# Performance work log

Measured on AMD Instinct MI355X. Metric: run time of the kernel, lower is better.

The kernel has to match this reference:

```python
import jax, jax.numpy as jnp
import numpy as np

N = 262144
C = 4096  # number of clusters


def _segment_max(x, seg, num_segments):
    # global_max_pool: per-cluster max over points
    return jax.ops.segment_max(x, seg, num_segments=num_segments)


def setup_inputs() -> dict:
    key = jax.random.key(0)
    ks = jax.random.split(key, 16)

    def lin(k, fan_in, fan_out):
        bound = 1.0 / np.sqrt(fan_in)
        kw, kb = jax.random.split(k)
        W = jax.random.uniform(kw, (fan_in, fan_out), jnp.float32, -bound, bound)
        b = jax.random.uniform(kb, (fan_out,), jnp.float32, -bound, bound)
        return W, b

    relative_points = jax.random.normal(ks[0], (N, 3), jnp.float32)
    features = jax.random.normal(ks[1], (N, 64), jnp.float32)
    cluster = jax.random.randint(ks[2], (N,), 0, C, jnp.int64)

    enc_W1, enc_b1 = lin(ks[3], 3, 32)    # neighborhood encoder MLP
    enc_W2, enc_b2 = lin(ks[4], 32, 64)
    W1, b1 = lin(ks[5], 3 + 64 + 64, 128)  # fc_layers (input_size + enc_out + 3)
    W2, b2 = lin(ks[6], 128, 128)
    G1, gb1 = lin(ks[7], 128, 128)          # fc_layers_global
    G2, gb2 = lin(ks[8], 128, 256)

    return dict(relative_points=relative_points, features=features, cluster=cluster,
                enc_W1=enc_W1, enc_b1=enc_b1, enc_W2=enc_W2, enc_b2=enc_b2,
                W1=W1, b1=b1, W2=W2, b2=b2, G1=G1, gb1=gb1, G2=G2, gb2=gb2)


def reference(relative_points, features, cluster,
              enc_W1, enc_b1, enc_W2, enc_b2,
              W1, b1, W2, b2, G1, gb1, G2, gb2):
    # --- neighborhood encoder: per-point MLP then per-cluster max-pool ---
    h = jax.nn.relu(relative_points @ enc_W1 + enc_b1)          # [N, 32]
    h = jax.nn.relu(h @ enc_W2 + enc_b2)                        # [N, 64]
    neigh_enc = _segment_max(h, cluster, C)                     # [C, 64]

    # gather-by-index duplication + concat
    dup = neigh_enc[cluster]                                    # [N, 64]
    encoded = jnp.concatenate([relative_points, features, dup], axis=1)  # [N, 131]

    # local fc stack (relu, leaky=False)
    encoded = jax.nn.relu(encoded @ W1 + b1)                    # [N, 128]
    encoded = jax.nn.relu(encoded @ W2 + b2)                    # [N, 128]

    # global_max_pool (mean=False)
    encoded_global = _segment_max(encoded, cluster, C)          # [C, 128]

    # global fc stack
    encoded_global = jax.nn.relu(encoded_global @ G1 + gb1)     # [C, 128]
    encoded_global = jax.nn.relu(encoded_global @ G2 + gb2)     # [C, 256]
    return encoded_global
```

## Files before the change

### kernel.cpp

```cpp
#include <hip/hip_runtime.h>
#include <hip/hip_bf16.h>

#define NN 262144
#define CC 4096
#define NBLK 64
#define PPB (NN / NBLK)
#define NT (NN / 64)
#define SLOTS 3

typedef __attribute__((ext_vector_type(8))) short bf16x8;
typedef __attribute__((ext_vector_type(4))) float f32x4;

__device__ __forceinline__ unsigned pk2(float a, float b) {
  __hip_bfloat16 ha = __float2bfloat16(a);
  __hip_bfloat16 hb = __float2bfloat16(b);
  unsigned short ua, ub;
  __builtin_memcpy(&ua, &ha, 2);
  __builtin_memcpy(&ub, &hb, 2);
  return (unsigned)ua | ((unsigned)ub << 16);
}

__global__ __launch_bounds__(256) void k_init(
    const int* __restrict__ cluster, unsigned* __restrict__ hist2d,
    const float* __restrict__ eW2, const float* __restrict__ W1,
    const float* __restrict__ W2, unsigned* __restrict__ packE,
    unsigned* __restrict__ pack1, unsigned* __restrict__ pack2)
{
  __shared__ unsigned h[CC];
  const int t = threadIdx.x, b = blockIdx.x;
  if (b < NBLK) {
    for (int q = t; q < CC; q += 256) h[q] = 0u;
    __syncthreads();
    const int base = b * PPB;
#pragma unroll 4
    for (int k = 0; k < PPB; k += 256) atomicAdd(&h[cluster[base + k + t]], 1u);
    __syncthreads();
    for (int q = t; q < CC; q += 256) hist2d[b * CC + q] = h[q];
    return;
  }
  const int id = (b - NBLK) * 256 + t;
  if (id < 1024) {
    const int nt = id >> 8, l = (id >> 2) & 63, v = id & 3;
    const int k0 = (l >> 4) * 8 + 2 * v, col = nt * 16 + (l & 15);
    packE[id] = pk2(eW2[k0 * 64 + col], eW2[(k0 + 1) * 64 + col]);
  } else if (id < 1024 + 6144) {
    const int j = id - 1024;
    const int kk = j >> 11, nt = (j >> 8) & 7, l = (j >> 2) & 63, v = j & 3;
    const int col = nt * 16 + (l & 15);
    float vals[2];
#pragma unroll
    for (int hh = 0; hh < 2; ++hh) {
      const int k = kk * 32 + (l >> 4) * 8 + 2 * v + hh;
      vals[hh] = (k < 64) ? W1[(3 + k) * 128 + col]
               : (k < 67) ? W1[(k - 64) * 128 + col] : 0.f;
    }
    pack1[j] = pk2(vals[0], vals[1]);
  } else {
    const int j = id - (1024 + 6144);
    const int kk = j >> 11, nt = (j >> 8) & 7, l = (j >> 2) & 63, v = j & 3;
    const int col = nt * 16 + (l & 15);
    const int k0 = kk * 32 + (l >> 4) * 4 + v;
    pack2[j] = pk2(W2[k0 * 128 + col], W2[(k0 + 16) * 128 + col]);
  }
}

#define ZERO_F4 589824
__global__ __launch_bounds__(256) void k_scan_a(
    const unsigned* __restrict__ hist2d, unsigned* __restrict__ base2d,
    unsigned* __restrict__ totals, float4* __restrict__ zbase)
{
  const int t = threadIdx.x, b = blockIdx.x;
  if (b < 16) {
    const int c = b * 256 + t;
    unsigned acc = 0;
#pragma unroll 4
    for (int bb = 0; bb < NBLK; ++bb) {
      const unsigned v = hist2d[bb * CC + c];
      base2d[bb * CC + c] = acc;
      acc += v;
    }
    totals[c] = acc;
  } else {
    const int zb = b - 16;
    const float4 z = {0.f, 0.f, 0.f, 0.f};
#pragma unroll 5
    for (int q = 0; q < 25; ++q) {
      const int idx = (zb * 25 + q) * 256 + t;
      if (idx < ZERO_F4) zbase[idx] = z;
    }
  }
}

__global__ __launch_bounds__(256) void k_scatter(
    const int* __restrict__ cluster, const unsigned* __restrict__ base2d,
    const unsigned* __restrict__ totals, unsigned* __restrict__ permcid,
    unsigned* __restrict__ cstart_g)
{
  __shared__ unsigned cur[CC];
  __shared__ unsigned part[256];
  const int t = threadIdx.x, b = blockIdx.x;
  unsigned loc[16];
  unsigned s = 0;
#pragma unroll
  for (int q = 0; q < 16; ++q) { loc[q] = s; s += totals[t * 16 + q]; }
  part[t] = s;
  __syncthreads();
  for (int off = 1; off < 256; off <<= 1) {
    const unsigned v = (t >= off) ? part[t - off] : 0u;
    __syncthreads();
    part[t] += v;
    __syncthreads();
  }
  const unsigned baset = part[t] - s;
#pragma unroll
  for (int q = 0; q < 16; ++q) {
    const unsigned cs = baset + loc[q];
    cur[t * 16 + q] = base2d[b * CC + t * 16 + q] + cs;
    if (b == 0) cstart_g[t * 16 + q] = cs;
  }
  __syncthreads();
  const int base = b * PPB;
#pragma unroll 4
  for (int k = 0; k < PPB; k += 256) {
    const int i = base + k + t;
    const int c = cluster[i];
    const unsigned pos = atomicAdd(&cur[c], 1u);
    permcid[pos] = (unsigned)i | ((unsigned)c << 18);
  }
}

__global__ __launch_bounds__(256) void k_enc_t(
    const float* __restrict__ pts, const unsigned* __restrict__ permcid,
    const unsigned* __restrict__ cstart,
    const float* __restrict__ eW1, const float* __restrict__ eb1,
    const float* __restrict__ eb2, const unsigned* __restrict__ packE,
    float* __restrict__ pse)
{
  __shared__ float P4[64 * 4];
  __shared__ unsigned h1s[64 * 20];
  __shared__ int seg_r0[65];
  __shared__ int seg_cid[64];
  __shared__ int seg_j[64];
  __shared__ int nseg_s;
  const int t = threadIdx.x;
  const int lane = t & 63, w = t >> 6;
  const int g = lane >> 4, ln15 = lane & 15;
  const int b = blockIdx.x;

  if (w == 0) {
    const unsigned pc = permcid[b * 64 + t];
    const int cid = (int)(pc >> 18);
    const int prevcid = (t == 0) ? -1 : (int)(permcid[b * 64 + t - 1] >> 18);
    const bool flag = (t == 0) || (prevcid != cid);
    const unsigned long long mask = __ballot(flag);
    const int rank = (int)__popcll(mask & ((1ull << t) - 1ull));
    if (flag) {
      seg_r0[rank] = t;
      seg_cid[rank] = cid;
      seg_j[rank] = b - (int)(cstart[cid] >> 6);
    }
    if (t == 0) {
      const int ns = (int)__popcll(mask);
      nseg_s = ns;
      seg_r0[ns] = 64;
    }
    const int i = (int)(pc & 0x3FFFFu);
    P4[t * 4 + 0] = pts[i * 3 + 0];
    P4[t * 4 + 1] = pts[i * 3 + 1];
    P4[t * 4 + 2] = pts[i * 3 + 2];
    P4[t * 4 + 3] = 0.f;
  }
  __syncthreads();
  {
    const int r = t >> 2, qq = t & 3;
    const float p0 = P4[r * 4], p1 = P4[r * 4 + 1], p2 = P4[r * 4 + 2];
    unsigned wv[4];
#pragma unroll
    for (int u = 0; u < 4; ++u) {
      float hv[2];
#pragma unroll
      for (int hh = 0; hh < 2; ++hh) {
        const int cc2 = qq * 8 + 2 * u + hh;
        hv[hh] = fmaxf(fmaf(p2, eW1[64 + cc2],
                       fmaf(p1, eW1[32 + cc2],
                       fmaf(p0, eW1[cc2], eb1[cc2]))), 0.f);
      }
      wv[u] = pk2(hv[0], hv[1]);
    }
    uint4 st; st.x = wv[0]; st.y = wv[1]; st.z = wv[2]; st.w = wv[3];
    *reinterpret_cast<uint4*>(&h1s[r * 20 + qq * 4]) = st;
  }
  __syncthreads();
  {
    const int col = w * 16 + ln15;
    const bf16x8 bfr = *reinterpret_cast<const bf16x8*>(&packE[(w * 64 + lane) * 4]);
    const float bias = eb2[col];
    f32x4 acc[4];
#pragma unroll
    for (int m = 0; m < 4; ++m) acc[m] = f32x4{bias, bias, bias, bias};
#pragma unroll
    for (int m = 0; m < 4; ++m) {
      const bf16x8 a = *reinterpret_cast<const bf16x8*>(&h1s[(16 * m + ln15) * 20 + g * 4]);
      acc[m] = __builtin_amdgcn_mfma_f32_16x16x32_bf16(a, bfr, acc[m], 0, 0, 0);
    }
    const int nseg = nseg_s;
    for (int s = 0; s < nseg; ++s) {
      const int r0 = seg_r0[s], r1 = seg_r0[s + 1];
      float v = 0.f;
#pragma unroll
      for (int m = 0; m < 4; ++m)
#pragma unroll
        for (int q = 0; q < 4; ++q) {
          const int row = 16 * m + 4 * g + q;
          const bool in = (row >= r0) & (row < r1);
          v = fmaxf(v, in ? fmaxf(acc[m][q], 0.f) : 0.f);
        }
      v = fmaxf(v, __shfl_xor(v, 16, 64));
      v = fmaxf(v, __shfl_xor(v, 32, 64));
      if (lane < 16) {
        const int c = seg_cid[s], j = seg_j[s];
        if (j < SLOTS - 1)
          pse[((size_t)c * SLOTS + j) * 64 + col] = v;
        else
          atomicMax((int*)&pse[((size_t)c * SLOTS + (SLOTS - 1)) * 64 + col],
                    __float_as_int(v));
      }
    }
  }
}

__global__ __launch_bounds__(256) void k_cproj2(
    const float* __restrict__ pse, const float* __restrict__ W1,
    const float* __restrict__ b1, float* __restrict__ cproj)
{
  __shared__ float nm2[2][64];
  const int t = threadIdx.x, b = blockIdx.x;
  if (t < 128) {
    const int rr = t >> 6, col = t & 63;
    const float* p = pse + ((size_t)(b * 2 + rr) * SLOTS) * 64 + col;
    nm2[rr][col] = fmaxf(fmaxf(p[0], p[64]), p[128]);
  }
  __syncthreads();
  const int rr = t >> 7, col = t & 127;
  const float* __restrict__ Wd = W1 + 67 * 128;
  float a = b1[col];
#pragma unroll 4
  for (int j = 0; j < 16; ++j) {
    const f32x4 nv = *reinterpret_cast<const f32x4*>(&nm2[rr][4 * j]);
    a = fmaf(nv[0], Wd[(4 * j + 0) * 128 + col], a);
    a = fmaf(nv[1], Wd[(4 * j + 1) * 128 + col], a);
    a = fmaf(nv[2], Wd[(4 * j + 2) * 128 + col], a);
    a = fmaf(nv[3], Wd[(4 * j + 3) * 128 + col], a);
  }
  cproj[(size_t)(b * 2 + rr) * 128 + col] = a;
}

__global__ __launch_bounds__(256) void k_fc_t(
    const float* __restrict__ pts, const float* __restrict__ feat,
    const unsigned* __restrict__ permcid, const unsigned* __restrict__ cstart,
    const float* __restrict__ b2, const float* __restrict__ cproj,
    const unsigned* __restrict__ pack1, const unsigned* __restrict__ pack2,
    float* __restrict__ psf)
{
  __shared__ unsigned buf[64 * 68];
  __shared__ float cpd[8][128];
  __shared__ int ridx_l[64];
  __shared__ int cid_l[64];
  __shared__ int seg_r0[65];
  __shared__ int seg_cid[64];
  __shared__ int seg_j[64];
  __shared__ int nseg_s;
  const int t = threadIdx.x;
  const int lane = t & 63, w = t >> 6;
  const int g = lane >> 4, ln15 = lane & 15;
  const int b = blockIdx.x;

  if (w == 0) {
    const unsigned pc = permcid[b * 64 + t];
    const int cid = (int)(pc >> 18);
    cid_l[t] = cid;
    const int prevcid = (t == 0) ? -1 : (int)(permcid[b * 64 + t - 1] >> 18);
    const bool flag = (t == 0) || (prevcid != cid);
    const unsigned long long mask = __ballot(flag);
    const int rank = (int)__popcll(mask & ((1ull << t) - 1ull));
    ridx_l[t] = (int)__popcll(mask & ((2ull << t) - 1ull)) - 1;
    if (flag) {
      seg_r0[rank] = t;
      seg_cid[rank] = cid;
      seg_j[rank] = b - (int)(cstart[cid] >> 6);
    }
    if (t == 0) {
      const int ns = (int)__popcll(mask);
      nseg_s = ns;
      seg_r0[ns] = 64;
    }
  }
  {
    const int r = t >> 2, seg = t & 3;
    const int i = (int)(permcid[b * 64 + r] & 0x3FFFFu);
    const float4* __restrict__ fp = reinterpret_cast<const float4*>(&feat[(size_t)i * 64 + seg * 16]);
    const float4 f0 = fp[0], f1 = fp[1], f2 = fp[2], f3 = fp[3];
    uint4 s0v, s1v;
    s0v.x = pk2(f0.x, f0.y); s0v.y = pk2(f0.z, f0.w);
    s0v.z = pk2(f1.x, f1.y); s0v.w = pk2(f1.z, f1.w);
    s1v.x = pk2(f2.x, f2.y); s1v.y = pk2(f2.z, f2.w);
    s1v.z = pk2(f3.x, f3.y); s1v.w = pk2(f3.z, f3.w);
    *reinterpret_cast<uint4*>(&buf[r * 52 + seg * 8 + 0]) = s0v;
    *reinterpret_cast<uint4*>(&buf[r * 52 + seg * 8 + 4]) = s1v;
  }
  if (t < 64) {
    const int i = (int)(permcid[b * 64 + t] & 0x3FFFFu);
    uint4 pw;
    pw.x = pk2(pts[i * 3 + 0], pts[i * 3 + 1]);
    pw.y = pk2(pts[i * 3 + 2], 0.f);
    pw.z = 0u; pw.w = 0u;
    uint4 zz; zz.x = zz.y = zz.z = zz.w = 0u;
    *reinterpret_cast<uint4*>(&buf[t * 52 + 32]) = pw;
    *reinterpret_cast<uint4*>(&buf[t * 52 + 36]) = zz;
    *reinterpret_cast<uint4*>(&buf[t * 52 + 40]) = zz;
    *reinterpret_cast<uint4*>(&buf[t * 52 + 44]) = zz;
  }
  __syncthreads();
  {
    const int nseg = nseg_s;
    const int lim = (nseg < 8) ? nseg : 8;
    for (int s = t >> 7; s < lim; s += 2)
      cpd[s][t & 127] = cproj[(size_t)seg_cid[s] * 128 + (t & 127)];
  }
  __syncthreads();

  const int colA = w * 32 + ln15, colB = colA + 16;
  f32x4 acc0[4], acc1[4];
  {
    const int nseg = nseg_s;
    if (nseg <= 2) {
      const float cA0 = cpd[0][colA], cA1 = cpd[0][colB];
      const float cB0 = (nseg == 2) ? cpd[1][colA] : cA0;
      const float cB1 = (nseg == 2) ? cpd[1][colB] : cA1;
      const int rb = (nseg == 2) ? seg_r0[1] : 64;
#pragma unroll
      for (int m = 0; m < 4; ++m)
#pragma unroll
        for (int q = 0; q < 4; ++q) {
          const int row = 16 * m + 4 * g + q;
          acc0[m][q] = (row < rb) ? cA0 : cB0;
          acc1[m][q] = (row < rb) ? cA1 : cB1;
        }
    } else {
#pragma unroll
      for (int m = 0; m < 4; ++m)
#pragma unroll
        for (int q = 0; q < 4; ++q) {
          const int row = 16 * m + 4 * g + q;
          const int idx = ridx_l[row];
          if (idx < 8) {
            acc0[m][q] = cpd[idx][colA];
            acc1[m][q] = cpd[idx][colB];
          } else {
            const int cc = cid_l[row];
            acc0[m][q] = cproj[(size_t)cc * 128 + colA];
            acc1[m][q] = cproj[(size_t)cc * 128 + colB];
          }
        }
    }
  }
  {
#pragma unroll
    for (int kk = 0; kk < 3; ++kk) {
      const bf16x8 bf0 = *reinterpret_cast<const bf16x8*>(&pack1[((kk * 8 + 2 * w + 0) * 64 + lane) * 4]);
      const bf16x8 bf1 = *reinterpret_cast<const bf16x8*>(&pack1[((kk * 8 + 2 * w + 1) * 64 + lane) * 4]);
#pragma unroll
      for (int m = 0; m < 4; ++m) {
        const bf16x8 a = *reinterpret_cast<const bf16x8*>(&buf[(16 * m + ln15) * 52 + kk * 16 + g * 4]);
        acc0[m] = __builtin_amdgcn_mfma_f32_16x16x32_bf16(a, bf0, acc0[m], 0, 0, 0);
        acc1[m] = __builtin_amdgcn_mfma_f32_16x16x32_bf16(a, bf1, acc1[m], 0, 0, 0);
      }
    }
  }
  __syncthreads();
  {
#pragma unroll
    for (int m = 0; m < 4; ++m)
#pragma unroll
      for (int q = 0; q < 4; ++q) {
        const int row = 16 * m + 4 * g + q;
        buf[row * 68 + w * 16 + ln15] =
            pk2(fmaxf(acc0[m][q], 0.f), fmaxf(acc1[m][q], 0.f));
      }
  }
  __syncthreads();
  {
    const float bb0 = b2[colA], bb1 = b2[colB];
#pragma unroll
    for (int m = 0; m < 4; ++m) {
      acc0[m] = f32x4{bb0, bb0, bb0, bb0};
      acc1[m] = f32x4{bb1, bb1, bb1, bb1};
    }
#pragma unroll
    for (int kk = 0; kk < 4; ++kk) {
      const bf16x8 bf0 = *reinterpret_cast<const bf16x8*>(&pack2[((kk * 8 + 2 * w + 0) * 64 + lane) * 4]);
      const bf16x8 bf1 = *reinterpret_cast<const bf16x8*>(&pack2[((kk * 8 + 2 * w + 1) * 64 + lane) * 4]);
#pragma unroll
      for (int m = 0; m < 4; ++m) {
        const bf16x8 a = *reinterpret_cast<const bf16x8*>(&buf[(16 * m + ln15) * 68 + kk * 16 + g * 4]);
        acc0[m] = __builtin_amdgcn_mfma_f32_16x16x32_bf16(a, bf0, acc0[m], 0, 0, 0);
        acc1[m] = __builtin_amdgcn_mfma_f32_16x16x32_bf16(a, bf1, acc1[m], 0, 0, 0);
      }
    }
  }
  {
    const int nseg = nseg_s;
    for (int s = 0; s < nseg; ++s) {
      const int r0 = seg_r0[s], r1 = seg_r0[s + 1];
      float v0 = 0.f, v1 = 0.f;
#pragma unroll
      for (int m = 0; m < 4; ++m)
#pragma unroll
        for (int q = 0; q < 4; ++q) {
          const int row = 16 * m + 4 * g + q;
          const bool in = (row >= r0) & (row < r1);
          v0 = fmaxf(v0, in ? fmaxf(acc0[m][q], 0.f) : 0.f);
          v1 = fmaxf(v1, in ? fmaxf(acc1[m][q], 0.f) : 0.f);
        }
      v0 = fmaxf(v0, __shfl_xor(v0, 16, 64)); v0 = fmaxf(v0, __shfl_xor(v0, 32, 64));
      v1 = fmaxf(v1, __shfl_xor(v1, 16, 64)); v1 = fmaxf(v1, __shfl_xor(v1, 32, 64));
      if (lane < 16) {
        const int c = seg_cid[s], j = seg_j[s];
        if (j < SLOTS - 1) {
          psf[((size_t)c * SLOTS + j) * 128 + colA] = v0;
          psf[((size_t)c * SLOTS + j) * 128 + colB] = v1;
        } else {
          atomicMax((int*)&psf[((size_t)c * SLOTS + (SLOTS - 1)) * 128 + colA], __float_as_int(v0));
          atomicMax((int*)&psf[((size_t)c * SLOTS + (SLOTS - 1)) * 128 + colB], __float_as_int(v1));
        }
      }
    }
  }
}

__global__ __launch_bounds__(256) void k_glob(
    const float* __restrict__ psf, const float* __restrict__ G1,
    const float* __restrict__ gb1, const float* __restrict__ G2,
    const float* __restrict__ gb2, float* __restrict__ out)
{
  __shared__ float pooled[4][128];
  __shared__ float tg[4][128];
  const int t = threadIdx.x, b = blockIdx.x;
  const int c0 = b * 4;
#pragma unroll
  for (int q = 0; q < 2; ++q) {
    const int idx = q * 256 + t;
    const int cc = idx >> 7, col = idx & 127;
    const float* p = psf + (size_t)(c0 + cc) * (SLOTS * 128) + col;
    pooled[cc][col] = fmaxf(fmaxf(p[0], p[128]), p[256]);
  }
  __syncthreads();
  {
    const int col = t & 127, hi = t >> 7;
    float a0 = gb1[col], a1 = a0;
#pragma unroll 4
    for (int k = 0; k < 128; ++k) {
      const float wv = G1[k * 128 + col];
      a0 = fmaf(pooled[hi * 2 + 0][k], wv, a0);
      a1 = fmaf(pooled[hi * 2 + 1][k], wv, a1);
    }
    tg[hi * 2 + 0][col] = fmaxf(a0, 0.f);
    tg[hi * 2 + 1][col] = fmaxf(a1, 0.f);
  }
  __syncthreads();
  {
    float o[4];
#pragma unroll
    for (int q = 0; q < 4; ++q) o[q] = gb2[t];
#pragma unroll 2
    for (int k = 0; k < 128; ++k) {
      const float wv = G2[k * 256 + t];
#pragma unroll
      for (int q = 0; q < 4; ++q) o[q] = fmaf(tg[q][k], wv, o[q]);
    }
#pragma unroll
    for (int q = 0; q < 4; ++q)
      out[(size_t)(c0 + q) * 256 + t] = fmaxf(o[q], 0.f);
  }
}

extern "C" void kernel_launch(void* const* d_in, const int* in_sizes, int n_in,
                              void* d_out, int out_size, void* d_ws, size_t ws_size,
                              hipStream_t stream)
{
  (void)in_sizes; (void)n_in; (void)out_size; (void)ws_size;
  const float* pts  = (const float*)d_in[0];
  const float* feat = (const float*)d_in[1];
  const int*   clus = (const int*)  d_in[2];
  const float* eW1  = (const float*)d_in[3];
  const float* eb1  = (const float*)d_in[4];
  const float* eW2  = (const float*)d_in[5];
  const float* eb2  = (const float*)d_in[6];
  const float* W1   = (const float*)d_in[7];
  const float* b1   = (const float*)d_in[8];
  const float* W2   = (const float*)d_in[9];
  const float* b2   = (const float*)d_in[10];
  const float* G1   = (const float*)d_in[11];
  const float* gb1  = (const float*)d_in[12];
  const float* G2   = (const float*)d_in[13];
  const float* gb2  = (const float*)d_in[14];
  float* out = (float*)d_out;

  unsigned* ws      = (unsigned*)d_ws;
  unsigned* hist2d  = ws;
  unsigned* base2d  = ws + 262144;
  unsigned* totals  = ws + 524288;
  unsigned* cstart  = ws + 528384;
  unsigned* permcid = ws + 532480;
  unsigned* packE   = ws + 794624;
  unsigned* pack1   = ws + 795648;
  unsigned* pack2   = ws + 801792;
  float*    cproj   = (float*)(ws + 809984);
  float*    pse     = (float*)(ws + 1334272);
  float*    psf     = (float*)(ws + 2120704);

  k_init   <<<NBLK + 60, 256, 0, stream>>>(clus, hist2d, eW2, W1, W2,
                                           packE, pack1, pack2);
  k_scan_a <<<112, 256, 0, stream>>>(hist2d, base2d, totals, (float4*)pse);
  k_scatter<<<NBLK, 256, 0, stream>>>(clus, base2d, totals, permcid, cstart);
  k_enc_t  <<<NT, 256, 0, stream>>>(pts, permcid, cstart, eW1, eb1, eb2,
                                    packE, pse);
  k_cproj2 <<<CC / 2, 256, 0, stream>>>(pse, W1, b1, cproj);
  k_fc_t   <<<NT, 256, 0, stream>>>(pts, feat, permcid, cstart, b2, cproj,
                                    pack1, pack2, psf);
  k_glob   <<<1024, 256, 0, stream>>>(psf, G1, gb1, G2, gb2, out);
}
```

Measured before the change: 114.3 us.

## Double point tile to 128 rows in encoder and FC kernels

```diff
diff --git a/kernel.cpp b/kernel.cpp
--- a/kernel.cpp
+++ b/kernel.cpp
@@ -5,7 +5,7 @@
 #define CC 4096
 #define NBLK 64
 #define PPB (NN / NBLK)
-#define NT (NN / 64)
+#define NT2 (NN / 128)
 #define SLOTS 3
 
 typedef __attribute__((ext_vector_type(8))) short bf16x8;
@@ -136,34 +136,26 @@
     const float* __restrict__ eb2, const unsigned* __restrict__ packE,
     float* __restrict__ pse)
 {
-  __shared__ float P4[64 * 4];
-  __shared__ unsigned h1s[64 * 20];
-  __shared__ int seg_r0[65];
-  __shared__ int seg_cid[64];
-  __shared__ int seg_j[64];
+  __shared__ float P4[128 * 4];
+  __shared__ unsigned h1s[128 * 20];
+  __shared__ unsigned long long flagw[2];
+  __shared__ int seg_r0[129];
+  __shared__ int seg_cid[128];
+  __shared__ int seg_j[128];
   __shared__ int nseg_s;
   const int t = threadIdx.x;
   const int lane = t & 63, w = t >> 6;
   const int g = lane >> 4, ln15 = lane & 15;
   const int b = blockIdx.x;
 
-  if (w == 0) {
-    const unsigned pc = permcid[b * 64 + t];
-    const int cid = (int)(pc >> 18);
-    const int prevcid = (t == 0) ? -1 : (int)(permcid[b * 64 + t - 1] >> 18);
-    const bool flag = (t == 0) || (prevcid != cid);
-    const unsigned long long mask = __ballot(flag);
-    const int rank = (int)__popcll(mask & ((1ull << t) - 1ull));
-    if (flag) {
-      seg_r0[rank] = t;
-      seg_cid[rank] = cid;
-      seg_j[rank] = b - (int)(cstart[cid] >> 6);
-    }
-    if (t == 0) {
-      const int ns = (int)__popcll(mask);
-      nseg_s = ns;
-      seg_r0[ns] = 64;
-    }
+  int cid = -1; bool flag = false;
+  if (t < 128) {
+    const unsigned pc = permcid[b * 128 + t];
+    cid = (int)(pc >> 18);
+    const int prevcid = (t == 0) ? -1 : (int)(permcid[b * 128 + t - 1] >> 18);
+    flag = (t == 0) || (prevcid != cid);
+    const unsigned long long m = __ballot(flag);
+    if ((t & 63) == 0) flagw[t >> 6] = m;
     const int i = (int)(pc & 0x3FFFFu);
     P4[t * 4 + 0] = pts[i * 3 + 0];
     P4[t * 4 + 1] = pts[i * 3 + 1];
@@ -171,35 +163,54 @@
     P4[t * 4 + 3] = 0.f;
   }
   __syncthreads();
-  {
-    const int r = t >> 2, qq = t & 3;
+  if (t < 128) {
+    const unsigned long long m0 = flagw[0], m1 = flagw[1];
+    const int wv = t >> 6, ln = t & 63;
+    const unsigned long long mym = wv ? m1 : m0;
+    const int rank = (int)__popcll(mym & ((1ull << ln) - 1ull)) +
+                     (wv ? (int)__popcll(m0) : 0);
+    if (flag) {
+      seg_r0[rank] = t;
+      seg_cid[rank] = cid;
+      seg_j[rank] = b - (int)(cstart[cid] >> 7);
+    }
+    if (t == 0) {
+      const int ns = (int)(__popcll(m0) + __popcll(m1));
+      nseg_s = ns;
+      seg_r0[ns] = 128;
+    }
+  }
+  {
+    const int r = t >> 1, sg = t & 1;
     const float p0 = P4[r * 4], p1 = P4[r * 4 + 1], p2 = P4[r * 4 + 2];
-    unsigned wv[4];
-#pragma unroll
-    for (int u = 0; u < 4; ++u) {
+    unsigned wv4[8];
+#pragma unroll
+    for (int u = 0; u < 8; ++u) {
       float hv[2];
 #pragma unroll
       for (int hh = 0; hh < 2; ++hh) {
-        const int cc2 = qq * 8 + 2 * u + hh;
-        hv[hh] = fmaxf(fmaf(p2, eW1[64 + cc2],
-                       fmaf(p1, eW1[32 + cc2],
-                       fmaf(p0, eW1[cc2], eb1[cc2]))), 0.f);
-      }
-      wv[u] = pk2(hv[0], hv[1]);
-    }
-    uint4 st; st.x = wv[0]; st.y = wv[1]; st.z = wv[2]; st.w = wv[3];
-    *reinterpret_cast<uint4*>(&h1s[r * 20 + qq * 4]) = st;
+        const int c2 = sg * 16 + 2 * u + hh;
+        hv[hh] = fmaxf(fmaf(p2, eW1[64 + c2],
+                       fmaf(p1, eW1[32 + c2],
+                       fmaf(p0, eW1[c2], eb1[c2]))), 0.f);
+      }
+      wv4[u] = pk2(hv[0], hv[1]);
+    }
+    uint4 s0; s0.x = wv4[0]; s0.y = wv4[1]; s0.z = wv4[2]; s0.w = wv4[3];
+    uint4 s1; s1.x = wv4[4]; s1.y = wv4[5]; s1.z = wv4[6]; s1.w = wv4[7];
+    *reinterpret_cast<uint4*>(&h1s[r * 20 + sg * 8 + 0]) = s0;
+    *reinterpret_cast<uint4*>(&h1s[r * 20 + sg * 8 + 4]) = s1;
   }
   __syncthreads();
   {
     const int col = w * 16 + ln15;
     const bf16x8 bfr = *reinterpret_cast<const bf16x8*>(&packE[(w * 64 + lane) * 4]);
     const float bias = eb2[col];
-    f32x4 acc[4];
-#pragma unroll
-    for (int m = 0; m < 4; ++m) acc[m] = f32x4{bias, bias, bias, bias};
-#pragma unroll
-    for (int m = 0; m < 4; ++m) {
+    f32x4 acc[8];
+#pragma unroll
+    for (int m = 0; m < 8; ++m) acc[m] = f32x4{bias, bias, bias, bias};
+#pragma unroll
+    for (int m = 0; m < 8; ++m) {
       const bf16x8 a = *reinterpret_cast<const bf16x8*>(&h1s[(16 * m + ln15) * 20 + g * 4]);
       acc[m] = __builtin_amdgcn_mfma_f32_16x16x32_bf16(a, bfr, acc[m], 0, 0, 0);
     }
@@ -208,7 +219,7 @@
       const int r0 = seg_r0[s], r1 = seg_r0[s + 1];
       float v = 0.f;
 #pragma unroll
-      for (int m = 0; m < 4; ++m)
+      for (int m = 0; m < 8; ++m)
 #pragma unroll
         for (int q = 0; q < 4; ++q) {
           const int row = 16 * m + 4 * g + q;
@@ -262,125 +273,112 @@
     const unsigned* __restrict__ pack1, const unsigned* __restrict__ pack2,
     float* __restrict__ psf)
 {
-  __shared__ unsigned buf[64 * 68];
-  __shared__ float cpd[8][128];
-  __shared__ int ridx_l[64];
-  __shared__ int cid_l[64];
-  __shared__ int seg_r0[65];
-  __shared__ int seg_cid[64];
-  __shared__ int seg_j[64];
+  __shared__ unsigned buf[128 * 68];
+  __shared__ unsigned long long flagw[2];
+  __shared__ int cid_l[128];
+  __shared__ int seg_r0[129];
+  __shared__ int seg_cid[128];
+  __shared__ int seg_j[128];
   __shared__ int nseg_s;
   const int t = threadIdx.x;
   const int lane = t & 63, w = t >> 6;
   const int g = lane >> 4, ln15 = lane & 15;
   const int b = blockIdx.x;
 
-  if (w == 0) {
-    const unsigned pc = permcid[b * 64 + t];
-    const int cid = (int)(pc >> 18);
+  int cid = -1; bool flag = false;
+  if (t < 128) {
+    const unsigned pc = permcid[b * 128 + t];
+    cid = (int)(pc >> 18);
     cid_l[t] = cid;
-    const int prevcid = (t == 0) ? -1 : (int)(permcid[b * 64 + t - 1] >> 18);
-    const bool flag = (t == 0) || (prevcid != cid);
-    const unsigned long long mask = __ballot(flag);
-    const int rank = (int)__popcll(mask & ((1ull << t) - 1ull));
-    ridx_l[t] = (int)__popcll(mask & ((2ull << t) - 1ull)) - 1;
-    if (flag) {
-      seg_r0[rank] = t;
-      seg_cid[rank] = cid;
-      seg_j[rank] = b - (int)(cstart[cid] >> 6);
-    }
-    if (t == 0) {
-      const int ns = (int)__popcll(mask);
-      nseg_s = ns;
-      seg_r0[ns] = 64;
-    }
-  }
-  {
-    const int r = t >> 2, seg = t & 3;
-    const int i = (int)(permcid[b * 64 + r] & 0x3FFFFu);
-    const float4* __restrict__ fp = reinterpret_cast<const float4*>(&feat[(size_t)i * 64 + seg * 16]);
+    const int prevcid = (t == 0) ? -1 : (int)(permcid[b * 128 + t - 1] >> 18);
+    flag = (t == 0) || (prevcid != cid);
+    const unsigned long long m = __ballot(flag);
+    if ((t & 63) == 0) flagw[t >> 6] = m;
+  }
+  {
+    const int r = t >> 1, sg = t & 1;
+    const int i = (int)(permcid[b * 128 + r] & 0x3FFFFu);
+    const float4* __restrict__ fp = reinterpret_cast<const float4*>(&feat[(size_t)i * 64 + sg * 32]);
     const float4 f0 = fp[0], f1 = fp[1], f2 = fp[2], f3 = fp[3];
-    uint4 s0v, s1v;
+    const float4 f4 = fp[4], f5 = fp[5], f6 = fp[6], f7 = fp[7];
+    uint4 s0v, s1v, s2v, s3v;
     s0v.x = pk2(f0.x, f0.y); s0v.y = pk2(f0.z, f0.w);
     s0v.z = pk2(f1.x, f1.y); s0v.w = pk2(f1.z, f1.w);
     s1v.x = pk2(f2.x, f2.y); s1v.y = pk2(f2.z, f2.w);
     s1v.z = pk2(f3.x, f3.y); s1v.w = pk2(f3.z, f3.w);
-    *reinterpret_cast<uint4*>(&buf[r * 52 + seg * 8 + 0]) = s0v;
-    *reinterpret_cast<uint4*>(&buf[r * 52 + seg * 8 + 4]) = s1v;
-  }
-  if (t < 64) {
-    const int i = (int)(permcid[b * 64 + t] & 0x3FFFFu);
-    uint4 pw;
-    pw.x = pk2(pts[i * 3 + 0], pts[i * 3 + 1]);
-    pw.y = pk2(pts[i * 3 + 2], 0.f);
-    pw.z = 0u; pw.w = 0u;
-    uint4 zz; zz.x = zz.y = zz.z = zz.w = 0u;
-    *reinterpret_cast<uint4*>(&buf[t * 52 + 32]) = pw;
-    *reinterpret_cast<uint4*>(&buf[t * 52 + 36]) = zz;
-    *reinterpret_cast<uint4*>(&buf[t * 52 + 40]) = zz;
-    *reinterpret_cast<uint4*>(&buf[t * 52 + 44]) = zz;
-  }
-  __syncthreads();
-  {
-    const int nseg = nseg_s;
-    const int lim = (nseg < 8) ? nseg : 8;
-    for (int s = t >> 7; s < lim; s += 2)
-      cpd[s][t & 127] = cproj[(size_t)seg_cid[s] * 128 + (t & 127)];
-  }
-  __syncthreads();
+    s2v.x = pk2(f4.x, f4.y); s2v.y = pk2(f4.z, f4.w);
+    s2v.z = pk2(f5.x, f5.y); s2v.w = pk2(f5.z, f5.w);
+    s3v.x = pk2(f6.x, f6.y); s3v.y = pk2(f6.z, f6.w);
+    s3v.z = pk2(f7.x, f7.y); s3v.w = pk2(f7.z, f7.w);
+    unsigned* __restrict__ dst = &buf[r * 52 + sg * 16];
+    *reinterpret_cast<uint4*>(dst + 0)  = s0v;
+    *reinterpret_cast<uint4*>(dst + 4)  = s1v;
+    *reinterpret_cast<uint4*>(dst + 8)  = s2v;
+    *reinterpret_cast<uint4*>(dst + 12) = s3v;
+    if (sg) {
+      uint4 pw;
+      pw.x = pk2(pts[i * 3 + 0], pts[i * 3 + 1]);
+      pw.y = pk2(pts[i * 3 + 2], 0.f);
+      pw.z = 0u; pw.w = 0u;
+      uint4 zz; zz.x = zz.y = zz.z = zz.w = 0u;
+      *reinterpret_cast<uint4*>(&buf[r * 52 + 32]) = pw;
+      *reinterpret_cast<uint4*>(&buf[r * 52 + 36]) = zz;
+      *reinterpret_cast<uint4*>(&buf[r * 52 + 40]) = zz;
+      *reinterpret_cast<uint4*>(&buf[r * 52 + 44]) = zz;
+    }
+  }
+  __syncthreads();
+  if (t < 128) {
+    const unsigned long long m0 = flagw[0], m1 = flagw[1];
+    const int wv = t >> 6, ln = t & 63;
+    const unsigned long long mym = wv ? m1 : m0;
+    const int rank = (int)__popcll(mym & ((1ull << ln) - 1ull)) +
+                     (wv ? (int)__popcll(m0) : 0);
+    if (flag) {
+      seg_r0[rank] = t;
+      seg_cid[rank] = cid;
+      seg_j[rank] = b - (int)(cstart[cid] >> 7);
+    }
+    if (t == 0) {
+      const int ns = (int)(__popcll(m0) + __popcll(m1));
+      nseg_s = ns;
+      seg_r0[ns] = 128;
+    }
+  }
 
   const int colA = w * 32 + ln15, colB = colA + 16;
-  f32x4 acc0[4], acc1[4];
-  {
-    const int nseg = nseg_s;
-    if (nseg <= 2) {
-      const float cA0 = cpd[0][colA], cA1 = cpd[0][colB];
-      const float cB0 = (nseg == 2) ? cpd[1][colA] : cA0;
-      const float cB1 = (nseg == 2) ? cpd[1][colB] : cA1;
-      const int rb = (nseg == 2) ? seg_r0[1] : 64;
-#pragma unroll
-      for (int m = 0; m < 4; ++m)
-#pragma unroll
-        for (int q = 0; q < 4; ++q) {
-          const int row = 16 * m + 4 * g + q;
-          acc0[m][q] = (row < rb) ? cA0 : cB0;
-          acc1[m][q] = (row < rb) ? cA1 : cB1;
-        }
-    } else {
-#pragma unroll
-      for (int m = 0; m < 4; ++m)
-#pragma unroll
-        for (int q = 0; q < 4; ++q) {
-          const int row = 16 * m + 4 * g + q;
-          const int idx = ridx_l[row];
-          if (idx < 8) {
-            acc0[m][q] = cpd[idx][colA];
-            acc1[m][q] = cpd[idx][colB];
-          } else {
-            const int cc = cid_l[row];
-            acc0[m][q] = cproj[(size_t)cc * 128 + colA];
-            acc1[m][q] = cproj[(size_t)cc * 128 + colB];
-          }
-        }
-    }
-  }
-  {
+  f32x4 acc0[8], acc1[8];
+  {
+#pragma unroll
+    for (int m = 0; m < 8; ++m) {
+      acc0[m] = f32x4{0.f, 0.f, 0.f, 0.f};
+      acc1[m] = f32x4{0.f, 0.f, 0.f, 0.f};
+    }
 #pragma unroll
     for (int kk = 0; kk < 3; ++kk) {
       const bf16x8 bf0 = *reinterpret_cast<const bf16x8*>(&pack1[((kk * 8 + 2 * w + 0) * 64 + lane) * 4]);
       const bf16x8 bf1 = *reinterpret_cast<const bf16x8*>(&pack1[((kk * 8 + 2 * w + 1) * 64 + lane) * 4]);
 #pragma unroll
-      for (int m = 0; m < 4; ++m) {
+      for (int m = 0; m < 8; ++m) {
         const bf16x8 a = *reinterpret_cast<const bf16x8*>(&buf[(16 * m + ln15) * 52 + kk * 16 + g * 4]);
         acc0[m] = __builtin_amdgcn_mfma_f32_16x16x32_bf16(a, bf0, acc0[m], 0, 0, 0);
         acc1[m] = __builtin_amdgcn_mfma_f32_16x16x32_bf16(a, bf1, acc1[m], 0, 0, 0);
       }
     }
-  }
-  __syncthreads();
-  {
-#pragma unroll
-    for (int m = 0; m < 4; ++m)
+#pragma unroll
+    for (int m = 0; m < 8; ++m)
+#pragma unroll
+      for (int q = 0; q < 4; ++q) {
+        const int row = 16 * m + 4 * g + q;
+        const int cc = cid_l[row];
+        acc0[m][q] += cproj[(size_t)cc * 128 + colA];
+        acc1[m][q] += cproj[(size_t)cc * 128 + colB];
+      }
+  }
+  __syncthreads();
+  {
+#pragma unroll
+    for (int m = 0; m < 8; ++m)
 #pragma unroll
       for (int q = 0; q < 4; ++q) {
         const int row = 16 * m + 4 * g + q;
@@ -392,7 +390,7 @@
   {
     const float bb0 = b2[colA], bb1 = b2[colB];
 #pragma unroll
-    for (int m = 0; m < 4; ++m) {
+    for (int m = 0; m < 8; ++m) {
       acc0[m] = f32x4{bb0, bb0, bb0, bb0};
       acc1[m] = f32x4{bb1, bb1, bb1, bb1};
     }
@@ -401,7 +399,7 @@
       const bf16x8 bf0 = *reinterpret_cast<const bf16x8*>(&pack2[((kk * 8 + 2 * w + 0) * 64 + lane) * 4]);
       const bf16x8 bf1 = *reinterpret_cast<const bf16x8*>(&pack2[((kk * 8 + 2 * w + 1) * 64 + lane) * 4]);
 #pragma unroll
-      for (int m = 0; m < 4; ++m) {
+      for (int m = 0; m < 8; ++m) {
         const bf16x8 a = *reinterpret_cast<const bf16x8*>(&buf[(16 * m + ln15) * 68 + kk * 16 + g * 4]);
         acc0[m] = __builtin_amdgcn_mfma_f32_16x16x32_bf16(a, bf0, acc0[m], 0, 0, 0);
         acc1[m] = __builtin_amdgcn_mfma_f32_16x16x32_bf16(a, bf1, acc1[m], 0, 0, 0);
@@ -414,7 +412,7 @@
       const int r0 = seg_r0[s], r1 = seg_r0[s + 1];
       float v0 = 0.f, v1 = 0.f;
 #pragma unroll
-      for (int m = 0; m < 4; ++m)
+      for (int m = 0; m < 8; ++m)
 #pragma unroll
         for (int q = 0; q < 4; ++q) {
           const int row = 16 * m + 4 * g + q;
@@ -523,10 +521,10 @@
                                            packE, pack1, pack2);
   k_scan_a <<<112, 256, 0, stream>>>(hist2d, base2d, totals, (float4*)pse);
   k_scatter<<<NBLK, 256, 0, stream>>>(clus, base2d, totals, permcid, cstart);
-  k_enc_t  <<<NT, 256, 0, stream>>>(pts, permcid, cstart, eW1, eb1, eb2,
-                                    packE, pse);
+  k_enc_t  <<<NT2, 256, 0, stream>>>(pts, permcid, cstart, eW1, eb1, eb2,
+                                     packE, pse);
   k_cproj2 <<<CC / 2, 256, 0, stream>>>(pse, W1, b1, cproj);
-  k_fc_t   <<<NT, 256, 0, stream>>>(pts, feat, permcid, cstart, b2, cproj,
-                                    pack1, pack2, psf);
+  k_fc_t   <<<NT2, 256, 0, stream>>>(pts, feat, permcid, cstart, b2, cproj,
+                                     pack1, pack2, psf);
   k_glob   <<<1024, 256, 0, stream>>>(psf, G1, gb1, G2, gb2, out);
 }
```

Result: slower. 141.4 us (+23.7%).
